# Kernel optimization log

Measured on AMD Instinct MI355X. Metric: run time of the kernel, lower is better.

Reference implementation:

```python
import jax, jax.numpy as jnp
import numpy as np

B, T, D, H, R = 64, 128, 128, 128, 4  # num_T == num_H == num_D forced by shape consistency
E = D * R  # SwiGLU expansion dim
EPS = 1e-5


def _pswiglu(x, Wu, bu, Wg, bg, Wd, bd):
    # x: [B,T,D]; per-token independent SwiGLU MLPs batched as one einsum
    up = jnp.einsum('btd,tde->bte', x, Wu) + bu          # [B,T,E]
    gate = jax.nn.silu(jnp.einsum('btd,tde->bte', x, Wg) + bg)
    return jnp.einsum('bte,ted->btd', up * gate, Wd) + bd  # [B,T,D]


def _rmsnorm(x, scale):
    rms = jnp.sqrt(jnp.mean(x * x, axis=-1, keepdims=True) + EPS)
    return x / rms * scale


def _token_mix(x, nT, nD, nH):
    # reshape (B,nT,nD)->(B,nT,nH,dk), transpose, merge -> (B,nH,nT*dk)
    dk = nD // nH
    b = x.shape[0]
    return x.reshape(b, nT, nH, dk).transpose(0, 2, 1, 3).reshape(b, nH, nT * dk)


def setup_inputs() -> dict:
    key = jax.random.key(0)
    ks = jax.random.split(key, 7)
    s = 0.02
    return {
        'x': jax.random.normal(ks[0], (B, T, D), dtype=jnp.float32),
        'W1_up': jax.random.normal(ks[1], (T, D, E), dtype=jnp.float32) * s,
        'b1_up': jnp.zeros((T, E), jnp.float32),
        'W1_gate': jax.random.normal(ks[2], (T, D, E), dtype=jnp.float32) * s,
        'b1_gate': jnp.zeros((T, E), jnp.float32),
        'W1_down': jax.random.normal(ks[3], (T, E, D), dtype=jnp.float32) * s,
        'b1_down': jnp.zeros((T, D), jnp.float32),
        'scale1': jnp.ones((D,), jnp.float32),
        'W2_up': jax.random.normal(ks[4], (T, D, E), dtype=jnp.float32) * s,
        'b2_up': jnp.zeros((T, E), jnp.float32),
        'W2_gate': jax.random.normal(ks[5], (T, D, E), dtype=jnp.float32) * s,
        'b2_gate': jnp.zeros((T, E), jnp.float32),
        'W2_down': jax.random.normal(ks[6], (T, E, D), dtype=jnp.float32) * s,
        'b2_down': jnp.zeros((T, D), jnp.float32),
        'scale2': jnp.ones((D,), jnp.float32),
    }


def reference(x, W1_up, b1_up, W1_gate, b1_gate, W1_down, b1_down, scale1,
              W2_up, b2_up, W2_gate, b2_gate, W2_down, b2_down, scale2):
    mixed = _token_mix(x, T, D, H)                         # [B,H,T*D/H] == [B,N,N]
    x1 = _rmsnorm(mixed + _pswiglu(mixed, W1_up, b1_up, W1_gate, b1_gate, W1_down, b1_down), scale1)
    rev = _token_mix(x1, T, H, D)                          # revert transpose
    out = _rmsnorm(rev + _pswiglu(rev, W2_up, b2_up, W2_gate, b2_gate, W2_down, b2_down), scale2)
    return out
```

## Files before the change

### kernel.cpp

```cpp
#include <hip/hip_runtime.h>

typedef __bf16 bf16x8 __attribute__((ext_vector_type(8)));
typedef float f32x4 __attribute__((ext_vector_type(4)));
typedef unsigned int uint;

#define XA_STR 152

union Frag { __bf16 b[8]; bf16x8 v; unsigned short u[8]; };

__device__ __forceinline__ unsigned short bfbits(float f) {
  union { __bf16 h; unsigned short s; } c; c.h = (__bf16)f; return c.s;
}
__device__ __forceinline__ float bf2f(unsigned short h) {
  return __uint_as_float(((uint)h) << 16);
}

#define GL1(dst, voff, base, IMM) \
  asm volatile("global_load_dword %0, %1, %2 offset:" #IMM : "=v"(dst) : "v"(voff), "s"(base))
#define GL4(dst, voff, base) \
  asm volatile("global_load_dwordx4 %0, %1, %2" : "=v"(dst) : "v"(voff), "s"(base))
#define WAITV(N) do { asm volatile("s_waitcnt vmcnt(" #N ")" ::: "memory"); \
  __builtin_amdgcn_sched_barrier(0); } while (0)
#define BARX() asm volatile("s_waitcnt lgkmcnt(0)\n\ts_barrier" ::: "memory")

__global__ __launch_bounds__(256) void transpose_in(const float* __restrict__ src,
                                                    unsigned short* __restrict__ dst) {
  __shared__ unsigned short tile[64][68];
  const int b  = blockIdx.x >> 2;
  const int f0 = ((blockIdx.x >> 1) & 1) * 64;
  const int s0 = (blockIdx.x & 1) * 64;
  const int j = threadIdx.x & 63, i0 = threadIdx.x >> 6;
  const float* sp = src + b * 16384 + f0 * 128 + s0 + j;
#pragma unroll
  for (int p = 0; p < 16; ++p) {
    const int i = i0 + p * 4;
    tile[i][j] = bfbits(sp[i * 128]);
  }
  __syncthreads();
  unsigned short* dp = dst + s0 * 8192 + b * 128 + f0 + j;
#pragma unroll
  for (int p = 0; p < 16; ++p) {
    const int i = i0 + p * 4;
    dp[(size_t)i * 8192] = tile[j][i];
  }
}

__global__ __launch_bounds__(512, 2) void mlp_main(
    const unsigned short* __restrict__ Xt,
    const float* __restrict__ Wu, const float* __restrict__ bu,
    const float* __restrict__ Wg, const float* __restrict__ bg,
    const float* __restrict__ Wd,
    unsigned short* __restrict__ partial)
{
  const int bid = blockIdx.x;
  const int s = bid >> 2, q = bid & 3;
  const int tid = threadIdx.x;
  const int wv = tid >> 6, lane = tid & 63;
  const int l16 = lane & 15, lg = lane >> 4;
  const int col = wv * 16 + l16;

  __shared__ __align__(16) unsigned short xa[64 * XA_STR];

  const float* WuS = Wu + (size_t)s * 65536;
  const float* WgS = Wg + (size_t)s * 65536;
  const float* WdS = Wd + (size_t)s * 65536;
  const unsigned short* XtS = Xt + (size_t)s * 8192;

  uint vu = (uint)(((lg * 8) * 512 + q * 128 + col) * 4);
  uint vd = (uint)(((q * 128 + lg * 8) * 128 + col) * 4);
  const uint vbo = (uint)((q * 128 + col) * 4);
  const uint vx0 = (uint)(tid * 16), vx1 = vx0 + 8192;

  float u0[8], g0[8], u1[8], g1[8], u2[8], g2[8], u3[8], g3[8];
  float d0[8], d1[8], d2[8], d3[8];
  f32x4 xq0, xq1;
  float buv, bgv;

#define ISSUE_UG(U, G) do { \
  GL1(U[0], vu, WuS, 0); GL1(U[1], vu, WuS, 2048); \
  GL1(G[0], vu, WgS, 0); GL1(G[1], vu, WgS, 2048); vu += 4096; \
  GL1(U[2], vu, WuS, 0); GL1(U[3], vu, WuS, 2048); \
  GL1(G[2], vu, WgS, 0); GL1(G[3], vu, WgS, 2048); vu += 4096; \
  GL1(U[4], vu, WuS, 0); GL1(U[5], vu, WuS, 2048); \
  GL1(G[4], vu, WgS, 0); GL1(G[5], vu, WgS, 2048); vu += 4096; \
  GL1(U[6], vu, WuS, 0); GL1(U[7], vu, WuS, 2048); \
  GL1(G[6], vu, WgS, 0); GL1(G[7], vu, WgS, 2048); vu += 53248; \
} while (0)

#define ISSUE_D(D) do { \
  GL1(D[0], vd, WdS, 0);    GL1(D[1], vd, WdS, 512); \
  GL1(D[2], vd, WdS, 1024); GL1(D[3], vd, WdS, 1536); \
  GL1(D[4], vd, WdS, 2048); GL1(D[5], vd, WdS, 2560); \
  GL1(D[6], vd, WdS, 3072); GL1(D[7], vd, WdS, 3584); vd += 16384; \
} while (0)

  Frag a[4];
#define LOADA(KK) do { \
  _Pragma("unroll") \
  for (int mt = 0; mt < 4; ++mt) \
    a[mt].v = *(const bf16x8*)&xa[(mt * 16 + l16) * XA_STR + (((KK) * 4 + lg) << 3)]; \
} while (0)

  f32x4 au[4] = {}, ag[4] = {}, ad[4] = {};
#define STEP_UG(U, G) do { \
  Frag fu, fg; \
  _Pragma("unroll") \
  for (int j = 0; j < 8; ++j) { fu.b[j] = (__bf16)U[j]; fg.b[j] = (__bf16)G[j]; } \
  _Pragma("unroll") \
  for (int mt = 0; mt < 4; ++mt) { \
    au[mt] = __builtin_amdgcn_mfma_f32_16x16x32_bf16(a[mt].v, fu.v, au[mt], 0, 0, 0); \
    ag[mt] = __builtin_amdgcn_mfma_f32_16x16x32_bf16(a[mt].v, fg.v, ag[mt], 0, 0, 0); } \
} while (0)

#define STEP_D(D) do { \
  Frag fd; \
  _Pragma("unroll") \
  for (int j = 0; j < 8; ++j) fd.b[j] = (__bf16)D[j]; \
  _Pragma("unroll") \
  for (int mt = 0; mt < 4; ++mt) \
    ad[mt] = __builtin_amdgcn_mfma_f32_16x16x32_bf16(a[mt].v, fd.v, ad[mt], 0, 0, 0); \
} while (0)

  GL4(xq0, vx0, XtS);
  GL4(xq1, vx1, XtS);
  GL1(buv, vbo, bu + s * 512, 0);
  GL1(bgv, vbo, bg + s * 512, 0);
  WAITV(0);
  {
    const int m0 = tid >> 4, ch0 = tid & 15;
    *(f32x4*)&xa[m0 * XA_STR + (ch0 << 3)] = xq0;
    const int p1 = tid + 512, m1 = p1 >> 4, ch1 = p1 & 15;
    *(f32x4*)&xa[m1 * XA_STR + (ch1 << 3)] = xq1;
  }
  BARX();

  ISSUE_UG(u0, g0);
  ISSUE_UG(u1, g1);
  ISSUE_UG(u2, g2);
  ISSUE_UG(u3, g3);
  ISSUE_D(d0);
  ISSUE_D(d1);
  ISSUE_D(d2);
  ISSUE_D(d3);

  WAITV(63); LOADA(0); STEP_UG(u0, g0);
  WAITV(63); LOADA(1); STEP_UG(u1, g1);
  WAITV(48); LOADA(2); STEP_UG(u2, g2);
  WAITV(32); LOADA(3); STEP_UG(u3, g3);

  float a2v[4][4];
#pragma unroll
  for (int mt = 0; mt < 4; ++mt)
#pragma unroll
    for (int r = 0; r < 4; ++r) {
      const float uv = au[mt][r] + buv;
      const float gv = ag[mt][r] + bgv;
      a2v[mt][r] = uv * (gv / (1.f + __expf(-gv)));
    }
  BARX();
#pragma unroll
  for (int mt = 0; mt < 4; ++mt)
#pragma unroll
    for (int r = 0; r < 4; ++r)
      xa[(mt * 16 + lg * 4 + r) * XA_STR + col] = bfbits(a2v[mt][r]);
  BARX();

  WAITV(24); LOADA(0); STEP_D(d0);
  WAITV(16); LOADA(1); STEP_D(d1);
  WAITV(8);  LOADA(2); STEP_D(d2);
  WAITV(0);  LOADA(3); STEP_D(d3);

  unsigned short* po = partial + (size_t)bid * 8192;
#pragma unroll
  for (int mt = 0; mt < 4; ++mt)
#pragma unroll
    for (int r = 0; r < 4; ++r)
      po[(mt * 16 + lg * 4 + r) * 128 + col] = bfbits(ad[mt][r]);

#undef ISSUE_UG
#undef ISSUE_D
#undef LOADA
#undef STEP_UG
#undef STEP_D
}

__global__ __launch_bounds__(256) void finish1(
    const unsigned short* __restrict__ part, const unsigned short* __restrict__ xt1,
    const float* __restrict__ bd, const float* __restrict__ scale,
    unsigned short* __restrict__ xt2)
{
  const int b = blockIdx.x >> 2, sq = blockIdx.x & 3;
  const int wvt = threadIdx.x >> 6, lane = threadIdx.x & 63;
  const int d0 = lane * 2;
  const float sc0 = scale[d0], sc1 = scale[d0 + 1];
  __shared__ unsigned short zt[128][40];

  for (int i = 0; i < 8; ++i) {
    const int sl = i * 4 + wvt;
    const int s = sq * 32 + sl;
    const uint rx = *(const uint*)(xt1 + (size_t)s * 8192 + b * 128 + d0);
    float z0 = bd[s * 128 + d0]     + bf2f((unsigned short)rx);
    float z1 = bd[s * 128 + d0 + 1] + bf2f((unsigned short)(rx >> 16));
#pragma unroll
    for (int p = 0; p < 4; ++p) {
      const uint rp = *(const uint*)(part + ((size_t)(s * 4 + p)) * 8192 + b * 128 + d0);
      z0 += bf2f((unsigned short)rp);
      z1 += bf2f((unsigned short)(rp >> 16));
    }
    float ss = z0 * z0 + z1 * z1;
#pragma unroll
    for (int off = 32; off; off >>= 1) ss += __shfl_xor(ss, off);
    const float inv = rsqrtf(ss * (1.f / 128.f) + 1e-5f);
    zt[d0][sl]     = bfbits(z0 * inv * sc0);
    zt[d0 + 1][sl] = bfbits(z1 * inv * sc1);
  }
  __syncthreads();
  const int dd = threadIdx.x >> 1, so = (threadIdx.x & 1) * 16;
  unsigned short* dst = xt2 + (size_t)dd * 8192 + b * 128 + sq * 32 + so;
  const uint4* srcv = (const uint4*)&zt[dd][so];
  ((uint4*)dst)[0] = srcv[0];
  ((uint4*)dst)[1] = srcv[1];
}

__global__ __launch_bounds__(256) void finish2(
    const unsigned short* __restrict__ part, const unsigned short* __restrict__ xt2,
    const float* __restrict__ bd, const float* __restrict__ scale,
    float* __restrict__ out)
{
  const int b = blockIdx.x >> 2, sq = blockIdx.x & 3;
  const int wvt = threadIdx.x >> 6, lane = threadIdx.x & 63;
  const int d0 = lane * 2;
  const float sc0 = scale[d0], sc1 = scale[d0 + 1];
  for (int i = 0; i < 8; ++i) {
    const int s = sq * 32 + i * 4 + wvt;
    const uint rx = *(const uint*)(xt2 + (size_t)s * 8192 + b * 128 + d0);
    float z0 = bd[s * 128 + d0]     + bf2f((unsigned short)rx);
    float z1 = bd[s * 128 + d0 + 1] + bf2f((unsigned short)(rx >> 16));
#pragma unroll
    for (int p = 0; p < 4; ++p) {
      const uint rp = *(const uint*)(part + ((size_t)(s * 4 + p)) * 8192 + b * 128 + d0);
      z0 += bf2f((unsigned short)rp);
      z1 += bf2f((unsigned short)(rp >> 16));
    }
    float ss = z0 * z0 + z1 * z1;
#pragma unroll
    for (int off = 32; off; off >>= 1) ss += __shfl_xor(ss, off);
    const float inv = rsqrtf(ss * (1.f / 128.f) + 1e-5f);
    *(float2*)(out + (size_t)b * 16384 + s * 128 + d0) =
        make_float2(z0 * inv * sc0, z1 * inv * sc1);
  }
}

extern "C" void kernel_launch(void* const* d_in, const int* in_sizes, int n_in,
                              void* d_out, int out_size, void* d_ws, size_t ws_size,
                              hipStream_t stream) {
  (void)in_sizes; (void)n_in; (void)out_size; (void)ws_size;
  const float* x   = (const float*)d_in[0];
  const float* W1u = (const float*)d_in[1];
  const float* b1u = (const float*)d_in[2];
  const float* W1g = (const float*)d_in[3];
  const float* b1g = (const float*)d_in[4];
  const float* W1d = (const float*)d_in[5];
  const float* b1d = (const float*)d_in[6];
  const float* sc1 = (const float*)d_in[7];
  const float* W2u = (const float*)d_in[8];
  const float* b2u = (const float*)d_in[9];
  const float* W2g = (const float*)d_in[10];
  const float* b2g = (const float*)d_in[11];
  const float* W2d = (const float*)d_in[12];
  const float* b2d = (const float*)d_in[13];
  const float* sc2 = (const float*)d_in[14];
  float* out = (float*)d_out;

  unsigned short* xt1  = (unsigned short*)d_ws;
  unsigned short* xt2  = xt1 + (size_t)1048576;
  unsigned short* part = xt2 + (size_t)1048576;

  transpose_in<<<256, 256, 0, stream>>>(x, xt1);
  mlp_main<<<512, 512, 0, stream>>>(xt1, W1u, b1u, W1g, b1g, W1d, part);
  finish1<<<256, 256, 0, stream>>>(part, xt1, b1d, sc1, xt2);
  mlp_main<<<512, 512, 0, stream>>>(xt2, W2u, b2u, W2g, b2g, W2d, part);
  finish2<<<256, 256, 0, stream>>>(part, xt2, b2d, sc2, out);
}
```

Measured before the change: 60.15 us.

## Stream MLP weights through a swizzled six-slot LDS ring via direct global-to-LDS loads

Replaces per-thread scalar global dword loads of the up, gate and down weights into registers with 16-byte global_load_lds transfers into a six-buffer shared-memory ring. An XOR swizzle is meant to avoid bank conflicts when B fragments are read back. Stages are refilled as they are consumed, with vmcnt waits and barriers between steps, and the down-projection weights are prefetched during the up/gate phase. This frees many VGPRs and widens memory requests. In exchange it adds about 96KB of LDS per block, which likely prevents the two-blocks-per-CU occupancy the launch bounds ask for, plus many extra block barriers.

New measurement: 65.29 us. +8.6%, slower.

```diff
diff --git a/kernel.cpp b/kernel.cpp
--- a/kernel.cpp
+++ b/kernel.cpp
@@ -59,40 +59,24 @@
   const int l16 = lane & 15, lg = lane >> 4;
   const int col = wv * 16 + l16;
 
+  __shared__ __align__(16) float wb[6][4096];
   __shared__ __align__(16) unsigned short xa[64 * XA_STR];
 
-  const float* WuS = Wu + (size_t)s * 65536;
-  const float* WgS = Wg + (size_t)s * 65536;
-  const float* WdS = Wd + (size_t)s * 65536;
-  const unsigned short* XtS = Xt + (size_t)s * 8192;
-
-  uint vu = (uint)(((lg * 8) * 512 + q * 128 + col) * 4);
-  uint vd = (uint)(((q * 128 + lg * 8) * 128 + col) * 4);
-  const uint vbo = (uint)((q * 128 + col) * 4);
-  const uint vx0 = (uint)(tid * 16), vx1 = vx0 + 8192;
-
-  float u0[8], g0[8], u1[8], g1[8], u2[8], g2[8], u3[8], g3[8];
-  float d0[8], d1[8], d2[8], d3[8];
-  f32x4 xq0, xq1;
-  float buv, bgv;
-
-#define ISSUE_UG(U, G) do { \
-  GL1(U[0], vu, WuS, 0); GL1(U[1], vu, WuS, 2048); \
-  GL1(G[0], vu, WgS, 0); GL1(G[1], vu, WgS, 2048); vu += 4096; \
-  GL1(U[2], vu, WuS, 0); GL1(U[3], vu, WuS, 2048); \
-  GL1(G[2], vu, WgS, 0); GL1(G[3], vu, WgS, 2048); vu += 4096; \
-  GL1(U[4], vu, WuS, 0); GL1(U[5], vu, WuS, 2048); \
-  GL1(G[4], vu, WgS, 0); GL1(G[5], vu, WgS, 2048); vu += 4096; \
-  GL1(U[6], vu, WuS, 0); GL1(U[7], vu, WuS, 2048); \
-  GL1(G[6], vu, WgS, 0); GL1(G[7], vu, WgS, 2048); vu += 53248; \
-} while (0)
-
-#define ISSUE_D(D) do { \
-  GL1(D[0], vd, WdS, 0);    GL1(D[1], vd, WdS, 512); \
-  GL1(D[2], vd, WdS, 1024); GL1(D[3], vd, WdS, 1536); \
-  GL1(D[4], vd, WdS, 2048); GL1(D[5], vd, WdS, 2560); \
-  GL1(D[6], vd, WdS, 3072); GL1(D[7], vd, WdS, 3584); vd += 16384; \
-} while (0)
+  const float* WuS = Wu + (size_t)s * 65536 + q * 128;
+  const float* WgS = Wg + (size_t)s * 65536 + q * 128;
+  const float* WdS = Wd + (size_t)s * 65536 + (size_t)q * 16384;
+
+  auto ISSUE = [&](const float* base, int rs, float* bb) {
+#pragma unroll
+    for (int r = 0; r < 2; ++r) {
+      const int p = (r << 9) + tid;
+      const int k = p >> 5, ch = p & 31;
+      const int chs = ch ^ (((k >> 3) & 1) << 2);
+      __builtin_amdgcn_global_load_lds(
+          (const __attribute__((address_space(1))) void*)(base + (size_t)k * rs + (chs << 2)),
+          (__attribute__((address_space(3))) void*)(bb + (p << 2)), 16, 0, 0);
+    }
+  };
 
   Frag a[4];
 #define LOADA(KK) do { \
@@ -101,74 +85,84 @@
     a[mt].v = *(const bf16x8*)&xa[(mt * 16 + l16) * XA_STR + (((KK) * 4 + lg) << 3)]; \
 } while (0)
 
+  const int cswz = col ^ ((lg & 1) << 4);
+  auto BFRAG = [&](const float* bb) {
+    Frag f;
+    const float* bp = bb + (lg << 3) * 128 + cswz;
+#pragma unroll
+    for (int j = 0; j < 8; ++j) f.b[j] = (__bf16)bp[j * 128];
+    return f;
+  };
+
   f32x4 au[4] = {}, ag[4] = {}, ad[4] = {};
-#define STEP_UG(U, G) do { \
-  Frag fu, fg; \
-  _Pragma("unroll") \
-  for (int j = 0; j < 8; ++j) { fu.b[j] = (__bf16)U[j]; fg.b[j] = (__bf16)G[j]; } \
-  _Pragma("unroll") \
-  for (int mt = 0; mt < 4; ++mt) { \
-    au[mt] = __builtin_amdgcn_mfma_f32_16x16x32_bf16(a[mt].v, fu.v, au[mt], 0, 0, 0); \
-    ag[mt] = __builtin_amdgcn_mfma_f32_16x16x32_bf16(a[mt].v, fg.v, ag[mt], 0, 0, 0); } \
-} while (0)
-
-#define STEP_D(D) do { \
-  Frag fd; \
-  _Pragma("unroll") \
-  for (int j = 0; j < 8; ++j) fd.b[j] = (__bf16)D[j]; \
+#define MFMA4(f, acc) do { \
   _Pragma("unroll") \
   for (int mt = 0; mt < 4; ++mt) \
-    ad[mt] = __builtin_amdgcn_mfma_f32_16x16x32_bf16(a[mt].v, fd.v, ad[mt], 0, 0, 0); \
+    acc[mt] = __builtin_amdgcn_mfma_f32_16x16x32_bf16(a[mt].v, f.v, acc[mt], 0, 0, 0); \
 } while (0)
 
-  GL4(xq0, vx0, XtS);
-  GL4(xq1, vx1, XtS);
-  GL1(buv, vbo, bu + s * 512, 0);
-  GL1(bgv, vbo, bg + s * 512, 0);
-  WAITV(0);
+  float buv, bgv;
+  f32x4 xq0, xq1;
+  const uint vbo = (uint)(col * 4);
+  const uint vx0 = (uint)(tid * 16), vx1 = vx0 + 8192;
+  GL1(buv, vbo, bu + s * 512 + q * 128, 0);
+  GL1(bgv, vbo, bg + s * 512 + q * 128, 0);
+  GL4(xq0, vx0, Xt + (size_t)s * 8192);
+  GL4(xq1, vx1, Xt + (size_t)s * 8192);
+  ISSUE(WuS,            512, wb[0]);
+  ISSUE(WgS,            512, wb[1]);
+  ISSUE(WuS + 32 * 512, 512, wb[2]);
+  ISSUE(WgS + 32 * 512, 512, wb[3]);
+  ISSUE(WuS + 64 * 512, 512, wb[4]);
+
+  WAITV(10);
   {
     const int m0 = tid >> 4, ch0 = tid & 15;
     *(f32x4*)&xa[m0 * XA_STR + (ch0 << 3)] = xq0;
     const int p1 = tid + 512, m1 = p1 >> 4, ch1 = p1 & 15;
     *(f32x4*)&xa[m1 * XA_STR + (ch1 << 3)] = xq1;
   }
-  BARX();
-
-  ISSUE_UG(u0, g0);
-  ISSUE_UG(u1, g1);
-  ISSUE_UG(u2, g2);
-  ISSUE_UG(u3, g3);
-  ISSUE_D(d0);
-  ISSUE_D(d1);
-  ISSUE_D(d2);
-  ISSUE_D(d3);
-
-  WAITV(63); LOADA(0); STEP_UG(u0, g0);
-  WAITV(63); LOADA(1); STEP_UG(u1, g1);
-  WAITV(48); LOADA(2); STEP_UG(u2, g2);
-  WAITV(32); LOADA(3); STEP_UG(u3, g3);
-
-  float a2v[4][4];
-#pragma unroll
-  for (int mt = 0; mt < 4; ++mt)
-#pragma unroll
-    for (int r = 0; r < 4; ++r) {
-      const float uv = au[mt][r] + buv;
-      const float gv = ag[mt][r] + bgv;
-      a2v[mt][r] = uv * (gv / (1.f + __expf(-gv)));
-    }
-  BARX();
-#pragma unroll
-  for (int mt = 0; mt < 4; ++mt)
-#pragma unroll
-    for (int r = 0; r < 4; ++r)
-      xa[(mt * 16 + lg * 4 + r) * XA_STR + col] = bfbits(a2v[mt][r]);
-  BARX();
-
-  WAITV(24); LOADA(0); STEP_D(d0);
-  WAITV(16); LOADA(1); STEP_D(d1);
-  WAITV(8);  LOADA(2); STEP_D(d2);
-  WAITV(0);  LOADA(3); STEP_D(d3);
+
+  WAITV(8); BARX(); ISSUE(WgS + 64 * 512, 512, wb[5]);
+  LOADA(0); { Frag f = BFRAG(wb[0]); MFMA4(f, au); }
+  WAITV(8); BARX(); ISSUE(WuS + 96 * 512, 512, wb[0]);
+  { Frag f = BFRAG(wb[1]); MFMA4(f, ag); }
+  WAITV(8); BARX(); ISSUE(WgS + 96 * 512, 512, wb[1]);
+  LOADA(1); { Frag f = BFRAG(wb[2]); MFMA4(f, au); }
+  WAITV(8); BARX(); ISSUE(WdS,            128, wb[2]);
+  { Frag f = BFRAG(wb[3]); MFMA4(f, ag); }
+  WAITV(8); BARX(); ISSUE(WdS + 32 * 128, 128, wb[3]);
+  LOADA(2); { Frag f = BFRAG(wb[4]); MFMA4(f, au); }
+  WAITV(8); BARX(); ISSUE(WdS + 64 * 128, 128, wb[4]);
+  { Frag f = BFRAG(wb[5]); MFMA4(f, ag); }
+  WAITV(8); BARX(); ISSUE(WdS + 96 * 128, 128, wb[5]);
+  LOADA(3); { Frag f = BFRAG(wb[0]); MFMA4(f, au); }
+  WAITV(8); BARX();
+  { Frag f = BFRAG(wb[1]); MFMA4(f, ag); }
+  {
+    float a2v[4][4];
+#pragma unroll
+    for (int mt = 0; mt < 4; ++mt)
+#pragma unroll
+      for (int r = 0; r < 4; ++r) {
+        const float uv = au[mt][r] + buv;
+        const float gv = ag[mt][r] + bgv;
+        a2v[mt][r] = uv * (gv / (1.f + __expf(-gv)));
+      }
+#pragma unroll
+    for (int mt = 0; mt < 4; ++mt)
+#pragma unroll
+      for (int r = 0; r < 4; ++r)
+        xa[(mt * 16 + lg * 4 + r) * XA_STR + col] = bfbits(a2v[mt][r]);
+  }
+  WAITV(6); BARX();
+  LOADA(0); { Frag f = BFRAG(wb[2]); MFMA4(f, ad); }
+  WAITV(4); BARX();
+  LOADA(1); { Frag f = BFRAG(wb[3]); MFMA4(f, ad); }
+  WAITV(2); BARX();
+  LOADA(2); { Frag f = BFRAG(wb[4]); MFMA4(f, ad); }
+  WAITV(0); BARX();
+  LOADA(3); { Frag f = BFRAG(wb[5]); MFMA4(f, ad); }
 
   unsigned short* po = partial + (size_t)bid * 8192;
 #pragma unroll
@@ -177,11 +171,8 @@
     for (int r = 0; r < 4; ++r)
       po[(mt * 16 + lg * 4 + r) * 128 + col] = bfbits(ad[mt][r]);
 
-#undef ISSUE_UG
-#undef ISSUE_D
 #undef LOADA
-#undef STEP_UG
-#undef STEP_D
+#undef MFMA4
 }
 
 __global__ __launch_bounds__(256) void finish1(
```

## Stream weights through LDS with triple-buffered global_load_lds and raise occupancy

Applied to the files above, without the earlier changes.

Replaces the register-resident prefetch of all up/gate/down weight fragments with a per-wave triple-buffered LDS ring filled by direct global-to-LDS loads. Each slot is read back, converted to bf16 and consumed by MFMAs while the next chunk is in flight. This frees the many VGPRs that held the weight prefetch, so launch bounds are raised to allow more blocks per CU. The cost is extra LDS traffic and capacity, plus a shallower in-flight window per wave, which depends on the extra occupancy to hide latency.

Result: no change. 59.80 us (-0.6%).

```diff
diff --git a/kernel.cpp b/kernel.cpp
--- a/kernel.cpp
+++ b/kernel.cpp
@@ -45,7 +45,7 @@
   }
 }
 
-__global__ __launch_bounds__(512, 2) void mlp_main(
+__global__ __launch_bounds__(512, 4) void mlp_main(
     const unsigned short* __restrict__ Xt,
     const float* __restrict__ Wu, const float* __restrict__ bu,
     const float* __restrict__ Wg, const float* __restrict__ bg,
@@ -59,39 +59,32 @@
   const int l16 = lane & 15, lg = lane >> 4;
   const int col = wv * 16 + l16;
 
+  __shared__ __align__(16) float wsl[8][3][512];
   __shared__ __align__(16) unsigned short xa[64 * XA_STR];
 
-  const float* WuS = Wu + (size_t)s * 65536;
-  const float* WgS = Wg + (size_t)s * 65536;
-  const float* WdS = Wd + (size_t)s * 65536;
-  const unsigned short* XtS = Xt + (size_t)s * 8192;
-
-  uint vu = (uint)(((lg * 8) * 512 + q * 128 + col) * 4);
-  uint vd = (uint)(((q * 128 + lg * 8) * 128 + col) * 4);
-  const uint vbo = (uint)((q * 128 + col) * 4);
-  const uint vx0 = (uint)(tid * 16), vx1 = vx0 + 8192;
-
-  float u0[8], g0[8], u1[8], g1[8], u2[8], g2[8], u3[8], g3[8];
-  float d0[8], d1[8], d2[8], d3[8];
-  f32x4 xq0, xq1;
-  float buv, bgv;
-
-#define ISSUE_UG(U, G) do { \
-  GL1(U[0], vu, WuS, 0); GL1(U[1], vu, WuS, 2048); \
-  GL1(G[0], vu, WgS, 0); GL1(G[1], vu, WgS, 2048); vu += 4096; \
-  GL1(U[2], vu, WuS, 0); GL1(U[3], vu, WuS, 2048); \
-  GL1(G[2], vu, WgS, 0); GL1(G[3], vu, WgS, 2048); vu += 4096; \
-  GL1(U[4], vu, WuS, 0); GL1(U[5], vu, WuS, 2048); \
-  GL1(G[4], vu, WgS, 0); GL1(G[5], vu, WgS, 2048); vu += 4096; \
-  GL1(U[6], vu, WuS, 0); GL1(U[7], vu, WuS, 2048); \
-  GL1(G[6], vu, WgS, 0); GL1(G[7], vu, WgS, 2048); vu += 53248; \
-} while (0)
-
-#define ISSUE_D(D) do { \
-  GL1(D[0], vd, WdS, 0);    GL1(D[1], vd, WdS, 512); \
-  GL1(D[2], vd, WdS, 1024); GL1(D[3], vd, WdS, 1536); \
-  GL1(D[4], vd, WdS, 2048); GL1(D[5], vd, WdS, 2560); \
-  GL1(D[6], vd, WdS, 3072); GL1(D[7], vd, WdS, 3584); vd += 16384; \
+  const float* WuS = Wu + (size_t)s * 65536 + q * 128 + wv * 16;
+  const float* WgS = Wg + (size_t)s * 65536 + q * 128 + wv * 16;
+  const float* WdS = Wd + (size_t)s * 65536 + (size_t)q * 16384 + wv * 16;
+
+  const int rlu = lg * 4096 + l16;
+  const int rld = lg * 1024 + l16;
+
+  float* const WA = &wsl[wv][0][0];
+  float* const WB = &wsl[wv][1][0];
+  float* const WC = &wsl[wv][2][0];
+
+#define ISSW(BASE, RS, OFF, SLOT) do { \
+  asm volatile("s_waitcnt lgkmcnt(0)" ::: "memory"); \
+  __builtin_amdgcn_sched_barrier(0); \
+  _Pragma("unroll") for (int i = 0; i < 8; ++i) \
+    __builtin_amdgcn_global_load_lds( \
+      (const __attribute__((address_space(1))) void*)((BASE) + (OFF) + i * (RS)), \
+      (__attribute__((address_space(3))) void*)((SLOT) + i * 64), 4, 0, 0); \
+} while (0)
+
+#define BS(SLOT, FR) do { \
+  _Pragma("unroll") for (int j = 0; j < 8; ++j) \
+    FR.b[j] = (__bf16)(SLOT)[j * 64 + (lg << 4) + l16]; \
 } while (0)
 
   Frag a[4];
@@ -102,30 +95,25 @@
 } while (0)
 
   f32x4 au[4] = {}, ag[4] = {}, ad[4] = {};
-#define STEP_UG(U, G) do { \
-  Frag fu, fg; \
-  _Pragma("unroll") \
-  for (int j = 0; j < 8; ++j) { fu.b[j] = (__bf16)U[j]; fg.b[j] = (__bf16)G[j]; } \
-  _Pragma("unroll") \
-  for (int mt = 0; mt < 4; ++mt) { \
-    au[mt] = __builtin_amdgcn_mfma_f32_16x16x32_bf16(a[mt].v, fu.v, au[mt], 0, 0, 0); \
-    ag[mt] = __builtin_amdgcn_mfma_f32_16x16x32_bf16(a[mt].v, fg.v, ag[mt], 0, 0, 0); } \
-} while (0)
-
-#define STEP_D(D) do { \
-  Frag fd; \
-  _Pragma("unroll") \
-  for (int j = 0; j < 8; ++j) fd.b[j] = (__bf16)D[j]; \
+#define MFMA4(FR, ACC) do { \
   _Pragma("unroll") \
   for (int mt = 0; mt < 4; ++mt) \
-    ad[mt] = __builtin_amdgcn_mfma_f32_16x16x32_bf16(a[mt].v, fd.v, ad[mt], 0, 0, 0); \
-} while (0)
-
-  GL4(xq0, vx0, XtS);
-  GL4(xq1, vx1, XtS);
+    ACC[mt] = __builtin_amdgcn_mfma_f32_16x16x32_bf16(a[mt].v, FR.v, ACC[mt], 0, 0, 0); \
+} while (0)
+
+  float buv, bgv;
+  f32x4 xq0, xq1;
+  const uint vbo = (uint)((q * 128 + col) * 4);
+  const uint vx0 = (uint)(tid * 16), vx1 = vx0 + 8192;
+  GL4(xq0, vx0, Xt + (size_t)s * 8192);
+  GL4(xq1, vx1, Xt + (size_t)s * 8192);
   GL1(buv, vbo, bu + s * 512, 0);
   GL1(bgv, vbo, bg + s * 512, 0);
-  WAITV(0);
+  ISSW(WuS, 512, rlu, WA);
+  ISSW(WgS, 512, rlu, WB);
+  ISSW(WuS + 16384, 512, rlu, WC);
+
+  WAITV(24);
   {
     const int m0 = tid >> 4, ch0 = tid & 15;
     *(f32x4*)&xa[m0 * XA_STR + (ch0 << 3)] = xq0;
@@ -134,19 +122,15 @@
   }
   BARX();
 
-  ISSUE_UG(u0, g0);
-  ISSUE_UG(u1, g1);
-  ISSUE_UG(u2, g2);
-  ISSUE_UG(u3, g3);
-  ISSUE_D(d0);
-  ISSUE_D(d1);
-  ISSUE_D(d2);
-  ISSUE_D(d3);
-
-  WAITV(63); LOADA(0); STEP_UG(u0, g0);
-  WAITV(63); LOADA(1); STEP_UG(u1, g1);
-  WAITV(48); LOADA(2); STEP_UG(u2, g2);
-  WAITV(32); LOADA(3); STEP_UG(u3, g3);
+  Frag f;
+  WAITV(16); LOADA(0); BS(WA, f); ISSW(WgS + 16384, 512, rlu, WA); MFMA4(f, au);
+  WAITV(16);           BS(WB, f); ISSW(WuS + 32768, 512, rlu, WB); MFMA4(f, ag);
+  WAITV(16); LOADA(1); BS(WC, f); ISSW(WgS + 32768, 512, rlu, WC); MFMA4(f, au);
+  WAITV(16);           BS(WA, f); ISSW(WuS + 49152, 512, rlu, WA); MFMA4(f, ag);
+  WAITV(16); LOADA(2); BS(WB, f); ISSW(WgS + 49152, 512, rlu, WB); MFMA4(f, au);
+  WAITV(16);           BS(WC, f); ISSW(WdS,         128, rld, WC); MFMA4(f, ag);
+  WAITV(16); LOADA(3); BS(WA, f); ISSW(WdS +  4096, 128, rld, WA); MFMA4(f, au);
+  WAITV(16);           BS(WB, f); ISSW(WdS +  8192, 128, rld, WB); MFMA4(f, ag);
 
   float a2v[4][4];
 #pragma unroll
@@ -165,10 +149,10 @@
       xa[(mt * 16 + lg * 4 + r) * XA_STR + col] = bfbits(a2v[mt][r]);
   BARX();
 
-  WAITV(24); LOADA(0); STEP_D(d0);
-  WAITV(16); LOADA(1); STEP_D(d1);
-  WAITV(8);  LOADA(2); STEP_D(d2);
-  WAITV(0);  LOADA(3); STEP_D(d3);
+  WAITV(16); LOADA(0); BS(WC, f); ISSW(WdS + 12288, 128, rld, WC); MFMA4(f, ad);
+  WAITV(16); LOADA(1); BS(WA, f); MFMA4(f, ad);
+  WAITV(8);  LOADA(2); BS(WB, f); MFMA4(f, ad);
+  WAITV(0);  LOADA(3); BS(WC, f); MFMA4(f, ad);
 
   unsigned short* po = partial + (size_t)bid * 8192;
 #pragma unroll
@@ -177,11 +161,10 @@
     for (int r = 0; r < 4; ++r)
       po[(mt * 16 + lg * 4 + r) * 128 + col] = bfbits(ad[mt][r]);
 
-#undef ISSUE_UG
-#undef ISSUE_D
+#undef ISSW
+#undef BS
 #undef LOADA
-#undef STEP_UG
-#undef STEP_D
+#undef MFMA4
 }
 
 __global__ __launch_bounds__(256) void finish1(
```
